# Kernel optimization log

Hardware: AMD Instinct MI355X
Metric: run time of the kernel (lower is better)

Reference implementation:

```python
import jax, jax.numpy as jnp
import numpy as np

B, F, V, E, T, NTOK, G, D = 8192, 64, 1000, 64, 2, 16, 4, 256
LN_EPS = 1e-5


def setup_inputs() -> dict:
    key = jax.random.key(0)
    ks = jax.random.split(key, 5)
    int_feats = jax.random.randint(ks[0], (B, F), 0, V, dtype=jnp.int64)
    missing_mask = jax.random.randint(ks[1], (B, F), 0, 2, dtype=jnp.int32)
    # deterministic seeded permutation of features split into NTOK equal groups
    perm = np.random.default_rng(1234).permutation(F)
    group_idx = jnp.asarray(perm.reshape(NTOK, G), dtype=jnp.int32)
    emb_tables = jax.random.normal(ks[2], (T, F, V, E), jnp.float32) * 0.02
    missing_emb = jax.random.normal(ks[3], (T, F, E), jnp.float32) * 0.02
    kW, kb = jax.random.split(ks[4])
    W = jax.random.normal(kW, (D, E * T), jnp.float32) * (1.0 / np.sqrt(E * T))
    b = jnp.zeros((D,), jnp.float32)
    ln_gamma = jnp.ones((D,), jnp.float32)
    ln_beta = jnp.zeros((D,), jnp.float32)
    return {"int_feats": int_feats, "missing_mask": missing_mask,
            "group_idx": group_idx, "emb_tables": emb_tables,
            "missing_emb": missing_emb, "W": W, "b": b,
            "ln_gamma": ln_gamma, "ln_beta": ln_beta}


def reference(int_feats, missing_mask, group_idx, emb_tables, missing_emb, W, b, ln_gamma, ln_beta):
    f_idx = jnp.arange(F)[None, :]  # (1, F) broadcast with (B, F) ids
    # per-table feature embedding gather: [T, B, F, E]
    feats = jax.vmap(lambda tbl: tbl[f_idx, int_feats])(emb_tables)
    # additive missing embeddings
    mask = missing_mask.astype(feats.dtype)
    feats = feats + mask[None, :, :, None] * missing_emb[:, None, :, :]
    # token-group mean pooling: [T, B, NTOK, G, E] -> [T, B, NTOK, E]
    pooled = feats[:, :, group_idx, :].mean(axis=3)
    # concat tables along feature dim (table order preserved): [B, NTOK, T*E]
    x = jnp.moveaxis(pooled, 0, 2).reshape(B, NTOK, T * E)
    # Linear -> SiLU -> LayerNorm
    h = jax.nn.silu(x @ W.T + b)
    mu = h.mean(-1, keepdims=True)
    var = ((h - mu) ** 2).mean(-1, keepdims=True)
    return (h - mu) * jax.lax.rsqrt(var + LN_EPS) * ln_gamma + ln_beta
```

## Files before the change

kernel.cpp:

```cpp
#include <hip/hip_runtime.h>
#include <math.h>

#define B_    8192
#define F_    64
#define V_    1000
#define E_    64
#define T_    2
#define NTOK_ 16
#define G_    4
#define D_    256
#define K_    128
#define LN_EPS 1e-5f

#define XSP   136

typedef __attribute__((ext_vector_type(8))) short  frag_ab;
typedef __attribute__((ext_vector_type(4))) float  frag_cd;

static __device__ __forceinline__ unsigned short f2bf(float f) {
    unsigned int u = __float_as_uint(f);
    u += 0x7FFFu + ((u >> 16) & 1u);
    return (unsigned short)(u >> 16);
}

__global__ __launch_bounds__(256) void convert_w_kernel(const float* __restrict__ W,
                                                        unsigned int* __restrict__ Wb_packed) {
    const int i = blockIdx.x * 256 + threadIdx.x;
    if (i < (D_ * K_) / 2) {
        const float2 v = *(const float2*)(W + (size_t)i * 2);
        Wb_packed[i] = (unsigned int)f2bf(v.x) | ((unsigned int)f2bf(v.y) << 16);
    }
}

__global__ __launch_bounds__(256) void fused_tokenizer_kernel(
    const int*   __restrict__ int_feats,
    const int*   __restrict__ missing_mask,
    const int*   __restrict__ group_idx,
    const float* __restrict__ emb_tables,
    const float* __restrict__ missing_emb,
    const unsigned short* __restrict__ Wb,
    const float* __restrict__ bias,
    const float* __restrict__ gamma,
    const float* __restrict__ beta,
    float*       __restrict__ out)
{
    __shared__ unsigned short xs[NTOK_][XSP];
    __shared__ float ps [NTOK_][4];
    __shared__ float pss[NTOK_][4];

    const int tid  = threadIdx.x;
    const int b    = blockIdx.x;
    const int lane = tid & 63;
    const int wave = tid >> 6;

    const int* __restrict__ feats_row = int_feats    + b * F_;
    const int* __restrict__ mask_row  = missing_mask + b * F_;

#pragma unroll
    for (int i = 0; i < 2; ++i) {
        const int c  = i * 256 + tid;
        const int n  = c >> 5;
        const int r4 = c & 31;
        const int t  = r4 >> 4;
        const int e  = (r4 & 15) * 4;
        const int4 fv = *(const int4*)(group_idx + n * G_);
        const int fs[4] = {fv.x, fv.y, fv.z, fv.w};
        float ax = 0.f, ay = 0.f, az = 0.f, aw = 0.f;
#pragma unroll
        for (int g = 0; g < G_; ++g) {
            const int f  = fs[g];
            const int id = feats_row[f];
            const float mk = (float)mask_row[f];
            const float4 v  = *(const float4*)(emb_tables + (((size_t)(t * F_ + f) * V_) + id) * E_ + e);
            const float4 mv = *(const float4*)(missing_emb + (size_t)(t * F_ + f) * E_ + e);
            ax += v.x + mk * mv.x;
            ay += v.y + mk * mv.y;
            az += v.z + mk * mv.z;
            aw += v.w + mk * mv.w;
        }
        union { unsigned int u[2]; } pk;
        pk.u[0] = (unsigned int)f2bf(0.25f * ax) | ((unsigned int)f2bf(0.25f * ay) << 16);
        pk.u[1] = (unsigned int)f2bf(0.25f * az) | ((unsigned int)f2bf(0.25f * aw) << 16);
        *(uint2*)(&xs[n][r4 * 4]) = make_uint2(pk.u[0], pk.u[1]);
    }
    __syncthreads();

    {
        const int m = lane & 15;
        const int q = lane >> 4;

        frag_ab a[4];
#pragma unroll
        for (int s = 0; s < 4; ++s)
            a[s] = *(const frag_ab*)(&xs[m][32 * s + 8 * q]);

        float h[4][4];
        float s_acc = 0.f, ss_acc = 0.f;

#pragma unroll
        for (int tt = 0; tt < 4; ++tt) {
            const int nt   = wave * 4 + tt;
            const int nrow = nt * 16 + m;
            const unsigned short* wp = Wb + (size_t)nrow * K_ + 8 * q;

            frag_cd acc = {0.f, 0.f, 0.f, 0.f};
#pragma unroll
            for (int s = 0; s < 4; ++s) {
                const frag_ab wfr = *(const frag_ab*)(wp + 32 * s);
                acc = __builtin_amdgcn_mfma_f32_16x16x32_bf16(wfr, a[s], acc, 0, 0, 0);
            }
            const float4 bn = *(const float4*)(bias + nt * 16 + q * 4);
            const float bnv[4] = {bn.x, bn.y, bn.z, bn.w};
#pragma unroll
            for (int reg = 0; reg < 4; ++reg) {
                const float z  = acc[reg] + bnv[reg];
                const float hh = z / (1.f + __expf(-z));
                h[tt][reg] = hh;
                s_acc  += hh;
                ss_acc += hh * hh;
            }
        }

        s_acc  += __shfl_xor(s_acc,  16, 64);
        ss_acc += __shfl_xor(ss_acc, 16, 64);
        s_acc  += __shfl_xor(s_acc,  32, 64);
        ss_acc += __shfl_xor(ss_acc, 32, 64);
        if (q == 0) { ps[m][wave] = s_acc; pss[m][wave] = ss_acc; }
    }
    __syncthreads();

    {
        const int m = lane & 15;
        const int q = lane >> 4;

        const float4 p4  = *(const float4*)(&ps[m][0]);
        const float4 pq4 = *(const float4*)(&pss[m][0]);
        const float s_tot  = (p4.x  + p4.y)  + (p4.z  + p4.w);
        const float ss_tot = (pq4.x + pq4.y) + (pq4.z + pq4.w);
        const float mu   = s_tot * (1.f / D_);
        const float var  = ss_tot * (1.f / D_) - mu * mu;
        const float rsig = rsqrtf(var + LN_EPS);

        float* __restrict__ orow = out + ((size_t)b * NTOK_ + m) * D_;

        (void)q; (void)orow;
    }

    {
    }
}

__global__ __launch_bounds__(256) void fused_tokenizer_kernel_v2(
    const int*   __restrict__ int_feats,
    const int*   __restrict__ missing_mask,
    const int*   __restrict__ group_idx,
    const float* __restrict__ emb_tables,
    const float* __restrict__ missing_emb,
    const unsigned short* __restrict__ Wb,
    const float* __restrict__ bias,
    const float* __restrict__ gamma,
    const float* __restrict__ beta,
    float*       __restrict__ out)
{
    __shared__ unsigned short xs[NTOK_][XSP];
    __shared__ float ps [NTOK_][4];
    __shared__ float pss[NTOK_][4];

    const int tid  = threadIdx.x;
    const int b    = blockIdx.x;
    const int lane = tid & 63;
    const int wave = tid >> 6;

    const int* __restrict__ feats_row = int_feats    + b * F_;
    const int* __restrict__ mask_row  = missing_mask + b * F_;

#pragma unroll
    for (int i = 0; i < 2; ++i) {
        const int c  = i * 256 + tid;
        const int n  = c >> 5;
        const int r4 = c & 31;
        const int t  = r4 >> 4;
        const int e  = (r4 & 15) * 4;
        const int4 fv = *(const int4*)(group_idx + n * G_);
        const int fs[4] = {fv.x, fv.y, fv.z, fv.w};
        float ax = 0.f, ay = 0.f, az = 0.f, aw = 0.f;
#pragma unroll
        for (int g = 0; g < G_; ++g) {
            const int f  = fs[g];
            const int id = feats_row[f];
            const float mk = (float)mask_row[f];
            const float4 v  = *(const float4*)(emb_tables + (((size_t)(t * F_ + f) * V_) + id) * E_ + e);
            const float4 mv = *(const float4*)(missing_emb + (size_t)(t * F_ + f) * E_ + e);
            ax += v.x + mk * mv.x;
            ay += v.y + mk * mv.y;
            az += v.z + mk * mv.z;
            aw += v.w + mk * mv.w;
        }
        union { unsigned int u[2]; } pk;
        pk.u[0] = (unsigned int)f2bf(0.25f * ax) | ((unsigned int)f2bf(0.25f * ay) << 16);
        pk.u[1] = (unsigned int)f2bf(0.25f * az) | ((unsigned int)f2bf(0.25f * aw) << 16);
        *(uint2*)(&xs[n][r4 * 4]) = make_uint2(pk.u[0], pk.u[1]);
    }
    __syncthreads();

    const int m = lane & 15;
    const int q = lane >> 4;

    frag_ab a[4];
#pragma unroll
    for (int s = 0; s < 4; ++s)
        a[s] = *(const frag_ab*)(&xs[m][32 * s + 8 * q]);

    float h[4][4];
    float s_acc = 0.f, ss_acc = 0.f;

#pragma unroll
    for (int tt = 0; tt < 4; ++tt) {
        const int nt   = wave * 4 + tt;
        const int nrow = nt * 16 + m;
        const unsigned short* wp = Wb + (size_t)nrow * K_ + 8 * q;

        frag_cd acc = {0.f, 0.f, 0.f, 0.f};
#pragma unroll
        for (int s = 0; s < 4; ++s) {
            const frag_ab wfr = *(const frag_ab*)(wp + 32 * s);
            acc = __builtin_amdgcn_mfma_f32_16x16x32_bf16(wfr, a[s], acc, 0, 0, 0);
        }
        const float4 bn = *(const float4*)(bias + nt * 16 + q * 4);
        const float bnv[4] = {bn.x, bn.y, bn.z, bn.w};
#pragma unroll
        for (int reg = 0; reg < 4; ++reg) {
            const float z  = acc[reg] + bnv[reg];
            const float hh = z / (1.f + __expf(-z));
            h[tt][reg] = hh;
            s_acc  += hh;
            ss_acc += hh * hh;
        }
    }

    s_acc  += __shfl_xor(s_acc,  16, 64);
    ss_acc += __shfl_xor(ss_acc, 16, 64);
    s_acc  += __shfl_xor(s_acc,  32, 64);
    ss_acc += __shfl_xor(ss_acc, 32, 64);
    if (q == 0) { ps[m][wave] = s_acc; pss[m][wave] = ss_acc; }
    __syncthreads();

    const float4 p4  = *(const float4*)(&ps[m][0]);
    const float4 pq4 = *(const float4*)(&pss[m][0]);
    const float s_tot  = (p4.x  + p4.y)  + (p4.z  + p4.w);
    const float ss_tot = (pq4.x + pq4.y) + (pq4.z + pq4.w);
    const float mu   = s_tot * (1.f / D_);
    const float var  = ss_tot * (1.f / D_) - mu * mu;
    const float rsig = rsqrtf(var + LN_EPS);

    float* __restrict__ orow = out + ((size_t)b * NTOK_ + m) * D_;
#pragma unroll
    for (int tt = 0; tt < 4; ++tt) {
        const int nt  = wave * 4 + tt;
        const int col = nt * 16 + q * 4;
        const float4 gm = *(const float4*)(gamma + col);
        const float4 bt = *(const float4*)(beta  + col);
        float4 o;
        o.x = (h[tt][0] - mu) * rsig * gm.x + bt.x;
        o.y = (h[tt][1] - mu) * rsig * gm.y + bt.y;
        o.z = (h[tt][2] - mu) * rsig * gm.z + bt.z;
        o.w = (h[tt][3] - mu) * rsig * gm.w + bt.w;
        *(float4*)(orow + col) = o;
    }
}

extern "C" void kernel_launch(void* const* d_in, const int* in_sizes, int n_in,
                              void* d_out, int out_size, void* d_ws, size_t ws_size,
                              hipStream_t stream) {
    const int*   int_feats    = (const int*)  d_in[0];
    const int*   missing_mask = (const int*)  d_in[1];
    const int*   group_idx    = (const int*)  d_in[2];
    const float* emb_tables   = (const float*)d_in[3];
    const float* missing_emb  = (const float*)d_in[4];
    const float* W            = (const float*)d_in[5];
    const float* bias         = (const float*)d_in[6];
    const float* gamma        = (const float*)d_in[7];
    const float* beta         = (const float*)d_in[8];
    float* out = (float*)d_out;

    unsigned short* Wb = (unsigned short*)d_ws;

    convert_w_kernel<<<(D_ * K_ / 2 + 255) / 256, 256, 0, stream>>>(W, (unsigned int*)Wb);
    fused_tokenizer_kernel_v2<<<B_, 256, 0, stream>>>(
        int_feats, missing_mask, group_idx, emb_tables, missing_emb,
        Wb, bias, gamma, beta, out);
}
```

Measured before the change: 256.8 us.

## Split fused tokenizer into gather-pool and MLP kernels via workspace buffer

When the workspace is large enough, the single fused kernel is replaced by two kernels: a gather/pool kernel that writes bf16 pooled tokens to global memory, and an MLP kernel that reads them back and does the matmul, SiLU and LayerNorm. Ids, masks and group indices are staged in shared memory, the missing-embedding load is skipped when the mask is zero, and outputs are staged through LDS so rows are written contiguously with nontemporal stores. The aim is to separate the latency-bound gather from the compute phase and to coalesce output writes. The cost is an extra global round-trip of the pooled activations and one more launch.

```diff
diff --git a/kernel.cpp b/kernel.cpp
--- a/kernel.cpp
+++ b/kernel.cpp
@@ -13,9 +13,11 @@
 #define LN_EPS 1e-5f
 
 #define XSP   136
+#define HSP   260
 
 typedef __attribute__((ext_vector_type(8))) short  frag_ab;
 typedef __attribute__((ext_vector_type(4))) float  frag_cd;
+typedef __attribute__((ext_vector_type(4))) float  f32x4;
 
 static __device__ __forceinline__ unsigned short f2bf(float f) {
     unsigned int u = __float_as_uint(f);
@@ -28,7 +30,153 @@
     const int i = blockIdx.x * 256 + threadIdx.x;
     if (i < (D_ * K_) / 2) {
         const float2 v = *(const float2*)(W + (size_t)i * 2);
-        Wb_packed[i] = (unsigned int)f2bf(v.x) | ((unsigned int)f2bf(v.y) << 16);
+        const unsigned int p = (unsigned int)f2bf(v.x) | ((unsigned int)f2bf(v.y) << 16);
+        __builtin_nontemporal_store(p, Wb_packed + i);
+    }
+}
+
+__global__ __launch_bounds__(256) void gather_pool_kernel(
+    const int*   __restrict__ int_feats,
+    const int*   __restrict__ missing_mask,
+    const int*   __restrict__ group_idx,
+    const float* __restrict__ emb_tables,
+    const float* __restrict__ missing_emb,
+    unsigned short* __restrict__ xout)
+{
+    __shared__ int sid[F_];
+    __shared__ int smask[F_];
+    __shared__ int sg[NTOK_ * G_];
+
+    const int tid = threadIdx.x;
+    const int b   = blockIdx.x;
+
+    if (tid < F_) {
+        sid[tid]   = int_feats[b * F_ + tid];
+        smask[tid] = missing_mask[b * F_ + tid];
+        sg[tid]    = group_idx[tid];
+    }
+    __syncthreads();
+
+#pragma unroll
+    for (int i = 0; i < 2; ++i) {
+        const int c  = i * 256 + tid;
+        const int n  = c >> 5;
+        const int r4 = c & 31;
+        const int t  = r4 >> 4;
+        const int e  = (r4 & 15) * 4;
+
+        float4 ev[G_], mv[G_];
+        float  mk[G_];
+#pragma unroll
+        for (int g = 0; g < G_; ++g) {
+            const int f  = sg[n * G_ + g];
+            const int id = sid[f];
+            ev[g] = *(const float4*)(emb_tables + (((size_t)(t * F_ + f) * V_) + id) * E_ + e);
+            mv[g] = *(const float4*)(missing_emb + (size_t)(t * F_ + f) * E_ + e);
+            mk[g] = (float)smask[f];
+        }
+        float ax = 0.f, ay = 0.f, az = 0.f, aw = 0.f;
+#pragma unroll
+        for (int g = 0; g < G_; ++g) {
+            ax += ev[g].x + mk[g] * mv[g].x;
+            ay += ev[g].y + mk[g] * mv[g].y;
+            az += ev[g].z + mk[g] * mv[g].z;
+            aw += ev[g].w + mk[g] * mv[g].w;
+        }
+        union { unsigned int u[2]; } pk;
+        pk.u[0] = (unsigned int)f2bf(0.25f * ax) | ((unsigned int)f2bf(0.25f * ay) << 16);
+        pk.u[1] = (unsigned int)f2bf(0.25f * az) | ((unsigned int)f2bf(0.25f * aw) << 16);
+        *(uint2*)(xout + ((size_t)b * NTOK_ + n) * K_ + r4 * 4) = make_uint2(pk.u[0], pk.u[1]);
+    }
+}
+
+__global__ __launch_bounds__(256) void mlp_kernel(
+    const unsigned short* __restrict__ xin,
+    const unsigned short* __restrict__ Wb,
+    const float* __restrict__ bias,
+    const float* __restrict__ gamma,
+    const float* __restrict__ beta,
+    float*       __restrict__ out)
+{
+    __shared__ float hs[NTOK_][HSP];
+    __shared__ float ps [NTOK_][4];
+    __shared__ float pss[NTOK_][4];
+
+    const int tid  = threadIdx.x;
+    const int b    = blockIdx.x;
+    const int lane = tid & 63;
+    const int wave = tid >> 6;
+
+    const int m = lane & 15;
+    const int q = lane >> 4;
+
+    const unsigned short* xrow = xin + ((size_t)b * NTOK_ + m) * K_ + 8 * q;
+    frag_ab a[4];
+#pragma unroll
+    for (int s = 0; s < 4; ++s)
+        a[s] = *(const frag_ab*)(xrow + 32 * s);
+
+    float h[4][4];
+    float s_acc = 0.f, ss_acc = 0.f;
+
+#pragma unroll
+    for (int tt = 0; tt < 4; ++tt) {
+        const int nt   = wave * 4 + tt;
+        const int nrow = nt * 16 + m;
+        const unsigned short* wp = Wb + (size_t)nrow * K_ + 8 * q;
+
+        frag_cd acc = {0.f, 0.f, 0.f, 0.f};
+#pragma unroll
+        for (int s = 0; s < 4; ++s) {
+            const frag_ab wfr = *(const frag_ab*)(wp + 32 * s);
+            acc = __builtin_amdgcn_mfma_f32_16x16x32_bf16(wfr, a[s], acc, 0, 0, 0);
+        }
+        const float4 bn = *(const float4*)(bias + nt * 16 + q * 4);
+        const float bnv[4] = {bn.x, bn.y, bn.z, bn.w};
+#pragma unroll
+        for (int reg = 0; reg < 4; ++reg) {
+            const float z  = acc[reg] + bnv[reg];
+            const float hh = z / (1.f + __expf(-z));
+            h[tt][reg] = hh;
+            s_acc  += hh;
+            ss_acc += hh * hh;
+        }
+    }
+
+    s_acc  += __shfl_xor(s_acc,  16, 64);
+    ss_acc += __shfl_xor(ss_acc, 16, 64);
+    s_acc  += __shfl_xor(s_acc,  32, 64);
+    ss_acc += __shfl_xor(ss_acc, 32, 64);
+    if (q == 0) { ps[m][wave] = s_acc; pss[m][wave] = ss_acc; }
+    __syncthreads();
+
+    const float4 p4  = *(const float4*)(&ps[m][0]);
+    const float4 pq4 = *(const float4*)(&pss[m][0]);
+    const float s_tot  = (p4.x  + p4.y)  + (p4.z  + p4.w);
+    const float ss_tot = (pq4.x + pq4.y) + (pq4.z + pq4.w);
+    const float mu   = s_tot * (1.f / D_);
+    const float var  = ss_tot * (1.f / D_) - mu * mu;
+    const float rsig = rsqrtf(var + LN_EPS);
+
+#pragma unroll
+    for (int tt = 0; tt < 4; ++tt) {
+        const int col = (wave * 4 + tt) * 16 + q * 4;
+        const float4 gm = *(const float4*)(gamma + col);
+        const float4 bt = *(const float4*)(beta  + col);
+        float4 o;
+        o.x = (h[tt][0] - mu) * rsig * gm.x + bt.x;
+        o.y = (h[tt][1] - mu) * rsig * gm.y + bt.y;
+        o.z = (h[tt][2] - mu) * rsig * gm.z + bt.z;
+        o.w = (h[tt][3] - mu) * rsig * gm.w + bt.w;
+        *(float4*)(&hs[m][col]) = o;
+    }
+    __syncthreads();
+
+#pragma unroll
+    for (int qq = 0; qq < 4; ++qq) {
+        const int n = wave * 4 + qq;
+        const f32x4 v = *(const f32x4*)(&hs[n][lane * 4]);
+        __builtin_nontemporal_store(v, (f32x4*)(out + ((size_t)b * NTOK_ + n) * D_ + lane * 4));
     }
 }
 
@@ -44,7 +192,13 @@
     const float* __restrict__ beta,
     float*       __restrict__ out)
 {
-    __shared__ unsigned short xs[NTOK_][XSP];
+    __shared__ __align__(16) char smem[NTOK_ * HSP * 4];
+    unsigned short (*xs)[XSP] = (unsigned short (*)[XSP])smem;
+    float          (*hs)[HSP] = (float (*)[HSP])smem;
+
+    __shared__ int   sid[F_];
+    __shared__ int   smask[F_];
+    __shared__ int   sg[NTOK_ * G_];
     __shared__ float ps [NTOK_][4];
     __shared__ float pss[NTOK_][4];
 
@@ -53,8 +207,12 @@
     const int lane = tid & 63;
     const int wave = tid >> 6;
 
-    const int* __restrict__ feats_row = int_feats    + b * F_;
-    const int* __restrict__ mask_row  = missing_mask + b * F_;
+    if (tid < F_) {
+        sid[tid]   = int_feats[b * F_ + tid];
+        smask[tid] = missing_mask[b * F_ + tid];
+        sg[tid]    = group_idx[tid];
+    }
+    __syncthreads();
 
 #pragma unroll
     for (int i = 0; i < 2; ++i) {
@@ -63,138 +221,18 @@
         const int r4 = c & 31;
         const int t  = r4 >> 4;
         const int e  = (r4 & 15) * 4;
-        const int4 fv = *(const int4*)(group_idx + n * G_);
-        const int fs[4] = {fv.x, fv.y, fv.z, fv.w};
         float ax = 0.f, ay = 0.f, az = 0.f, aw = 0.f;
 #pragma unroll
         for (int g = 0; g < G_; ++g) {
-            const int f  = fs[g];
-            const int id = feats_row[f];
-            const float mk = (float)mask_row[f];
-            const float4 v  = *(const float4*)(emb_tables + (((size_t)(t * F_ + f) * V_) + id) * E_ + e);
-            const float4 mv = *(const float4*)(missing_emb + (size_t)(t * F_ + f) * E_ + e);
-            ax += v.x + mk * mv.x;
-            ay += v.y + mk * mv.y;
-            az += v.z + mk * mv.z;
-            aw += v.w + mk * mv.w;
-        }
-        union { unsigned int u[2]; } pk;
-        pk.u[0] = (unsigned int)f2bf(0.25f * ax) | ((unsigned int)f2bf(0.25f * ay) << 16);
-        pk.u[1] = (unsigned int)f2bf(0.25f * az) | ((unsigned int)f2bf(0.25f * aw) << 16);
-        *(uint2*)(&xs[n][r4 * 4]) = make_uint2(pk.u[0], pk.u[1]);
-    }
-    __syncthreads();
-
-    {
-        const int m = lane & 15;
-        const int q = lane >> 4;
-
-        frag_ab a[4];
-#pragma unroll
-        for (int s = 0; s < 4; ++s)
-            a[s] = *(const frag_ab*)(&xs[m][32 * s + 8 * q]);
-
-        float h[4][4];
-        float s_acc = 0.f, ss_acc = 0.f;
-
-#pragma unroll
-        for (int tt = 0; tt < 4; ++tt) {
-            const int nt   = wave * 4 + tt;
-            const int nrow = nt * 16 + m;
-            const unsigned short* wp = Wb + (size_t)nrow * K_ + 8 * q;
-
-            frag_cd acc = {0.f, 0.f, 0.f, 0.f};
-#pragma unroll
-            for (int s = 0; s < 4; ++s) {
-                const frag_ab wfr = *(const frag_ab*)(wp + 32 * s);
-                acc = __builtin_amdgcn_mfma_f32_16x16x32_bf16(wfr, a[s], acc, 0, 0, 0);
+            const int f  = sg[n * G_ + g];
+            const int id = sid[f];
+            const float4 v = *(const float4*)(emb_tables + (((size_t)(t * F_ + f) * V_) + id) * E_ + e);
+            float vx = v.x, vy = v.y, vz = v.z, vw = v.w;
+            if (smask[f]) {
+                const float4 mv = *(const float4*)(missing_emb + (size_t)(t * F_ + f) * E_ + e);
+                vx += mv.x; vy += mv.y; vz += mv.z; vw += mv.w;
             }
-            const float4 bn = *(const float4*)(bias + nt * 16 + q * 4);
-            const float bnv[4] = {bn.x, bn.y, bn.z, bn.w};
-#pragma unroll
-            for (int reg = 0; reg < 4; ++reg) {
-                const float z  = acc[reg] + bnv[reg];
-                const float hh = z / (1.f + __expf(-z));
-                h[tt][reg] = hh;
-                s_acc  += hh;
-                ss_acc += hh * hh;
-            }
-        }
-
-        s_acc  += __shfl_xor(s_acc,  16, 64);
-        ss_acc += __shfl_xor(ss_acc, 16, 64);
-        s_acc  += __shfl_xor(s_acc,  32, 64);
-        ss_acc += __shfl_xor(ss_acc, 32, 64);
-        if (q == 0) { ps[m][wave] = s_acc; pss[m][wave] = ss_acc; }
-    }
-    __syncthreads();
-
-    {
-        const int m = lane & 15;
-        const int q = lane >> 4;
-
-        const float4 p4  = *(const float4*)(&ps[m][0]);
-        const float4 pq4 = *(const float4*)(&pss[m][0]);
-        const float s_tot  = (p4.x  + p4.y)  + (p4.z  + p4.w);
-        const float ss_tot = (pq4.x + pq4.y) + (pq4.z + pq4.w);
-        const float mu   = s_tot * (1.f / D_);
-        const float var  = ss_tot * (1.f / D_) - mu * mu;
-        const float rsig = rsqrtf(var + LN_EPS);
-
-        float* __restrict__ orow = out + ((size_t)b * NTOK_ + m) * D_;
-
-        (void)q; (void)orow;
-    }
-
-    {
-    }
-}
-
-__global__ __launch_bounds__(256) void fused_tokenizer_kernel_v2(
-    const int*   __restrict__ int_feats,
-    const int*   __restrict__ missing_mask,
-    const int*   __restrict__ group_idx,
-    const float* __restrict__ emb_tables,
-    const float* __restrict__ missing_emb,
-    const unsigned short* __restrict__ Wb,
-    const float* __restrict__ bias,
-    const float* __restrict__ gamma,
-    const float* __restrict__ beta,
-    float*       __restrict__ out)
-{
-    __shared__ unsigned short xs[NTOK_][XSP];
-    __shared__ float ps [NTOK_][4];
-    __shared__ float pss[NTOK_][4];
-
-    const int tid  = threadIdx.x;
-    const int b    = blockIdx.x;
-    const int lane = tid & 63;
-    const int wave = tid >> 6;
-
-    const int* __restrict__ feats_row = int_feats    + b * F_;
-    const int* __restrict__ mask_row  = missing_mask + b * F_;
-
-#pragma unroll
-    for (int i = 0; i < 2; ++i) {
-        const int c  = i * 256 + tid;
-        const int n  = c >> 5;
-        const int r4 = c & 31;
-        const int t  = r4 >> 4;
-        const int e  = (r4 & 15) * 4;
-        const int4 fv = *(const int4*)(group_idx + n * G_);
-        const int fs[4] = {fv.x, fv.y, fv.z, fv.w};
-        float ax = 0.f, ay = 0.f, az = 0.f, aw = 0.f;
-#pragma unroll
-        for (int g = 0; g < G_; ++g) {
-            const int f  = fs[g];
-            const int id = feats_row[f];
-            const float mk = (float)mask_row[f];
-            const float4 v  = *(const float4*)(emb_tables + (((size_t)(t * F_ + f) * V_) + id) * E_ + e);
-            const float4 mv = *(const float4*)(missing_emb + (size_t)(t * F_ + f) * E_ + e);
-            ax += v.x + mk * mv.x;
-            ay += v.y + mk * mv.y;
-            az += v.z + mk * mv.z;
-            aw += v.w + mk * mv.w;
+            ax += vx; ay += vy; az += vz; aw += vw;
         }
         union { unsigned int u[2]; } pk;
         pk.u[0] = (unsigned int)f2bf(0.25f * ax) | ((unsigned int)f2bf(0.25f * ay) << 16);
@@ -253,11 +291,9 @@
     const float var  = ss_tot * (1.f / D_) - mu * mu;
     const float rsig = rsqrtf(var + LN_EPS);
 
-    float* __restrict__ orow = out + ((size_t)b * NTOK_ + m) * D_;
 #pragma unroll
     for (int tt = 0; tt < 4; ++tt) {
-        const int nt  = wave * 4 + tt;
-        const int col = nt * 16 + q * 4;
+        const int col = (wave * 4 + tt) * 16 + q * 4;
         const float4 gm = *(const float4*)(gamma + col);
         const float4 bt = *(const float4*)(beta  + col);
         float4 o;
@@ -265,7 +301,15 @@
         o.y = (h[tt][1] - mu) * rsig * gm.y + bt.y;
         o.z = (h[tt][2] - mu) * rsig * gm.z + bt.z;
         o.w = (h[tt][3] - mu) * rsig * gm.w + bt.w;
-        *(float4*)(orow + col) = o;
+        *(float4*)(&hs[m][col]) = o;
+    }
+    __syncthreads();
+
+#pragma unroll
+    for (int qq = 0; qq < 4; ++qq) {
+        const int n = wave * 4 + qq;
+        const f32x4 v = *(const f32x4*)(&hs[n][lane * 4]);
+        __builtin_nontemporal_store(v, (f32x4*)(out + ((size_t)b * NTOK_ + n) * D_ + lane * 4));
     }
 }
 
@@ -284,9 +328,19 @@
     float* out = (float*)d_out;
 
     unsigned short* Wb = (unsigned short*)d_ws;
+    const size_t wb_bytes = (size_t)D_ * K_ * 2;
+    const size_t x_bytes  = (size_t)B_ * NTOK_ * K_ * 2;
+    unsigned short* x = (unsigned short*)((char*)d_ws + wb_bytes);
 
     convert_w_kernel<<<(D_ * K_ / 2 + 255) / 256, 256, 0, stream>>>(W, (unsigned int*)Wb);
-    fused_tokenizer_kernel_v2<<<B_, 256, 0, stream>>>(
-        int_feats, missing_mask, group_idx, emb_tables, missing_emb,
-        Wb, bias, gamma, beta, out);
-}
+
+    if (ws_size >= wb_bytes + x_bytes) {
+        gather_pool_kernel<<<B_, 256, 0, stream>>>(
+            int_feats, missing_mask, group_idx, emb_tables, missing_emb, x);
+        mlp_kernel<<<B_, 256, 0, stream>>>(x, Wb, bias, gamma, beta, out);
+    } else {
+        fused_tokenizer_kernel<<<B_, 256, 0, stream>>>(
+            int_feats, missing_mask, group_idx, emb_tables, missing_emb,
+            Wb, bias, gamma, beta, out);
+    }
+}
```

Measured after the change: 275.9 us. 7.4% more time.
